# Kernel tuning notes

Measured on AMD Instinct MI355X. Metric: run time of the kernel, lower is better.

The kernel has to match this reference:

```python
import jax, jax.numpy as jnp
import numpy as np

N_NODES = 50000
N_EDGES = 800000
IN_DIM = 128
ATT_DIM = 128
NEG_SLOPE = 0.01  # nn.LeakyReLU default


def setup_inputs() -> dict:
    key = jax.random.key(0)
    ks = jax.random.split(key, 8)
    x = jax.random.normal(ks[0], (N_NODES, IN_DIM), dtype=jnp.float32)
    src_idx = jax.random.randint(ks[1], (N_EDGES,), 0, N_NODES, dtype=jnp.int32)
    dst_idx = jax.random.randint(ks[2], (N_EDGES,), 0, N_NODES, dtype=jnp.int32)
    # small init scale keeps exp(score) numerically tame
    src_w = jax.random.normal(ks[3], (IN_DIM, ATT_DIM), dtype=jnp.float32) * 0.05
    src_b = jnp.zeros((ATT_DIM,), dtype=jnp.float32)
    dst_w = jax.random.normal(ks[4], (IN_DIM, ATT_DIM), dtype=jnp.float32) * 0.05
    dst_b = jnp.zeros((ATT_DIM,), dtype=jnp.float32)
    att_w = jax.random.normal(ks[5], (ATT_DIM, 1), dtype=jnp.float32) * 0.05
    att_b = jnp.zeros((1,), dtype=jnp.float32)
    return {"x": x, "src_idx": src_idx, "dst_idx": dst_idx,
            "src_w": src_w, "src_b": src_b, "dst_w": dst_w, "dst_b": dst_b,
            "att_w": att_w, "att_b": att_b}


def reference(x, src_idx, dst_idx, src_w, src_b, dst_w, dst_b, att_w, att_b):
    n = x.shape[0]
    # 1) mean aggregation of source features onto destinations (copy_u + mean)
    deg = jax.ops.segment_sum(jnp.ones_like(dst_idx, dtype=x.dtype), dst_idx, num_segments=n)
    h_mean = jax.ops.segment_sum(x[src_idx], dst_idx, num_segments=n)
    h_mean = h_mean / jnp.maximum(deg, 1.0)[:, None]
    # 2) attention projections on nodes (dense GEMMs)
    ha_src = x @ src_w + src_b          # [N, att_dim]
    ha_dst = h_mean @ dst_w + dst_b     # [N, att_dim]
    # 3) per-edge u_add_v -> LeakyReLU -> att Linear -> exp
    e = jax.nn.leaky_relu(ha_src[src_idx] + ha_dst[dst_idx], NEG_SLOPE)  # [E, att_dim]
    s = jnp.exp(e @ att_w + att_b)      # [E, 1]
    # 4) edge softmax: normalize by segment sum over destination
    denom = jax.ops.segment_sum(s, dst_idx, num_segments=n)  # [N, 1]
    a = s / denom[dst_idx]              # [E, 1]
    # 5) u_mul_e weighted aggregation (sum)
    out = jax.ops.segment_sum(x[src_idx] * a, dst_idx, num_segments=n)  # [N, in_dim]
    return out
```

## Files before the change

kernel.cpp:

```cpp
#include <hip/hip_runtime.h>
#include <math.h>

#define N_NODES 50000
#define N_EDGES 800000
#define DIM 128
#define NEG_SLOPE 0.01f
#define CAP 64

typedef short v8s __attribute__((ext_vector_type(8)));
typedef float v4f __attribute__((ext_vector_type(4)));

__device__ inline unsigned f2bf2(float a, float b) {
    unsigned ua = __float_as_uint(a);
    unsigned ub = __float_as_uint(b);
    ua = (ua + 0x7fffu + ((ua >> 16) & 1u)) >> 16;
    ub = (ub + 0x7fffu + ((ub >> 16) & 1u)) & 0xffff0000u;
    return ua | ub;
}
__device__ inline float2 bf2f(unsigned u) {
    float2 r;
    r.x = __uint_as_float(u << 16);
    r.y = __uint_as_float(u & 0xffff0000u);
    return r;
}

__global__ __launch_bounds__(256) void k_prepw(
    const float* __restrict__ src_w, const float* __restrict__ dst_w,
    unsigned* __restrict__ whT, int* __restrict__ deg)
{
    int gid = blockIdx.x * 256 + threadIdx.x;
    if (gid < 256 * 64) {
        int n = gid >> 6;
        int kk = gid & 63;
        const float* W = (n < 128) ? src_w : dst_w;
        int col = n & 127;
        float w0 = W[(2 * kk) * DIM + col];
        float w1 = W[(2 * kk + 1) * DIM + col];
        whT[gid] = f2bf2(w0, w1);
    }
    if (gid < N_NODES) deg[gid] = 0;
}

__global__ __launch_bounds__(256) void k_scatter(
    const int* __restrict__ src, const int* __restrict__ dst,
    int* __restrict__ deg, int* __restrict__ slots)
{
    int e = blockIdx.x * 256 + threadIdx.x;
    if (e >= N_EDGES) return;
    int d = dst[e];
    int pos = atomicAdd(&deg[d], 1);
    if (pos < CAP) slots[d * CAP + pos] = src[e] * 64;
}

__global__ __launch_bounds__(256) void k_gemm(
    const float* __restrict__ x, const unsigned* __restrict__ whT,
    const float* __restrict__ src_b, unsigned* __restrict__ hx_u,
    unsigned* __restrict__ yu)
{
    __shared__ unsigned lds[64][196];
    int wave = threadIdx.x >> 6;
    int lane = threadIdx.x & 63;
    int quad = lane >> 4;
    int m = lane & 15;
    int m0 = blockIdx.x * 64 + wave * 16;
    int arow = m0 + m;
    int lr = wave * 16 + m;
    bool live = (arow < N_NODES);

    v8s b[4];
    #pragma unroll
    for (int k0 = 0; k0 < 4; ++k0) {
        float4 f0 = make_float4(0.f, 0.f, 0.f, 0.f);
        float4 f1 = f0;
        if (live) {
            const float4* xp = (const float4*)(x + (size_t)arow * DIM + k0 * 32 + quad * 8);
            f0 = xp[0];
            f1 = xp[1];
        }
        union { unsigned u[4]; v8s s; } pk;
        pk.u[0] = f2bf2(f0.x, f0.y);
        pk.u[1] = f2bf2(f0.z, f0.w);
        pk.u[2] = f2bf2(f1.x, f1.y);
        pk.u[3] = f2bf2(f1.z, f1.w);
        b[k0] = pk.s;
        int c = k0 * 32 + quad * 8 + 1;
        lds[lr][c + 0] = pk.u[0];
        lds[lr][c + 2] = pk.u[1];
        lds[lr][c + 4] = pk.u[2];
        lds[lr][c + 6] = pk.u[3];
    }

    #pragma unroll
    for (int nt = 0; nt < 16; ++nt) {
        v4f acc = {0.f, 0.f, 0.f, 0.f};
        const uint4* ap = (const uint4*)(whT + (size_t)(nt * 16 + m) * 64 + quad * 4);
        #pragma unroll
        for (int k0 = 0; k0 < 4; ++k0) {
            union { uint4 u; v8s s; } af;
            af.u = ap[k0 * 4];
            acc = __builtin_amdgcn_mfma_f32_16x16x32_bf16(af.s, b[k0], acc, 0, 0, 0);
        }
        if (nt < 8) {
            float4 bia = ((const float4*)src_b)[nt * 4 + quad];
            int c = nt * 16 + quad * 4;
            lds[lr][c]     = f2bf2(acc[0] + bia.x, acc[1] + bia.y);
            lds[lr][c + 2] = f2bf2(acc[2] + bia.z, acc[3] + bia.w);
        } else {
            int c = 64 + nt * 8 + quad * 2;
            lds[lr][c]     = f2bf2(acc[0], acc[1]);
            lds[lr][c + 1] = f2bf2(acc[2], acc[3]);
        }
    }
    __syncthreads();

    int rbase = blockIdx.x * 64;
    for (int i = threadIdx.x; i < 64 * 32; i += 256) {
        int r = i >> 5, c = i & 31;
        int row = rbase + r;
        if (row < N_NODES)
            ((uint4*)(hx_u + (size_t)row * 128))[c] = *(const uint4*)&lds[r][c * 4];
    }
    for (int i = threadIdx.x; i < 64 * 16; i += 256) {
        int r = i >> 4, c = i & 15;
        int row = rbase + r;
        if (row < N_NODES)
            ((uint4*)(yu + (size_t)row * 64))[c] = *(const uint4*)&lds[r][128 + c * 4];
    }
}

__global__ __launch_bounds__(256) void k_fuse(
    const uint2* __restrict__ hx, const unsigned* __restrict__ yu,
    const int* __restrict__ slots, const int* __restrict__ deg,
    const float* __restrict__ dst_b, const float* __restrict__ att_w,
    const float* __restrict__ att_b, float* __restrict__ out)
{
    int g = blockIdx.x * 256 + threadIdx.x;
    int node = g >> 6;
    int lane = g & 63;
    int grp = lane >> 4;
    int sl = lane & 15;
    int cnt = deg[node];
    if (cnt == 0) {
        if (grp < 2)
            ((float4*)out)[node * 32 + 2 * sl + grp] = make_float4(0.f, 0.f, 0.f, 0.f);
        return;
    }
    const int* sp = slots + node * CAP;

    float hd[8] = {0.f, 0.f, 0.f, 0.f, 0.f, 0.f, 0.f, 0.f};
    for (int i = grp; i < cnt; i += 4) {
        int off = sp[i];
        uint4 q = *((const uint4*)(yu + off) + sl);
        float2 f;
        f = bf2f(q.x); hd[0] += f.x; hd[1] += f.y;
        f = bf2f(q.y); hd[2] += f.x; hd[3] += f.y;
        f = bf2f(q.z); hd[4] += f.x; hd[5] += f.y;
        f = bf2f(q.w); hd[6] += f.x; hd[7] += f.y;
    }
    float inv = 1.0f / (float)cnt;
    float4 db0 = ((const float4*)dst_b)[2 * sl];
    float4 db1 = ((const float4*)dst_b)[2 * sl + 1];
    #pragma unroll
    for (int j = 0; j < 8; ++j) {
        hd[j] += __shfl_xor(hd[j], 32);
        hd[j] += __shfl_xor(hd[j], 16);
        hd[j] *= inv;
    }
    hd[0] += db0.x; hd[1] += db0.y; hd[2] += db0.z; hd[3] += db0.w;
    hd[4] += db1.x; hd[5] += db1.y; hd[6] += db1.z; hd[7] += db1.w;

    float4 aw0 = ((const float4*)att_w)[2 * sl];
    float4 aw1 = ((const float4*)att_w)[2 * sl + 1];
    float ab = att_b[0];
    float o[8] = {0.f, 0.f, 0.f, 0.f, 0.f, 0.f, 0.f, 0.f};
    float dsum = 0.f;
    for (int i = grp; i < cnt; i += 4) {
        int off = sp[i];
        const uint4* hp = (const uint4*)(hx + off);
        uint4 qa = hp[2 * sl];
        uint4 qb = hp[2 * sl + 1];
        float2 h01 = bf2f(qa.x), h23 = bf2f(qa.z);
        float2 h45 = bf2f(qb.x), h67 = bf2f(qb.z);
        float v, p;
        v = h01.x + hd[0]; v = (v > 0.f) ? v : v * NEG_SLOPE; p  = v * aw0.x;
        v = h01.y + hd[1]; v = (v > 0.f) ? v : v * NEG_SLOPE; p += v * aw0.y;
        v = h23.x + hd[2]; v = (v > 0.f) ? v : v * NEG_SLOPE; p += v * aw0.z;
        v = h23.y + hd[3]; v = (v > 0.f) ? v : v * NEG_SLOPE; p += v * aw0.w;
        v = h45.x + hd[4]; v = (v > 0.f) ? v : v * NEG_SLOPE; p += v * aw1.x;
        v = h45.y + hd[5]; v = (v > 0.f) ? v : v * NEG_SLOPE; p += v * aw1.y;
        v = h67.x + hd[6]; v = (v > 0.f) ? v : v * NEG_SLOPE; p += v * aw1.z;
        v = h67.y + hd[7]; v = (v > 0.f) ? v : v * NEG_SLOPE; p += v * aw1.w;
        p += __shfl_xor(p, 8);
        p += __shfl_xor(p, 4);
        p += __shfl_xor(p, 2);
        p += __shfl_xor(p, 1);
        float s = __expf(p + ab);
        float2 x01 = bf2f(qa.y), x23 = bf2f(qa.w);
        float2 x45 = bf2f(qb.y), x67 = bf2f(qb.w);
        o[0] += s * x01.x; o[1] += s * x01.y;
        o[2] += s * x23.x; o[3] += s * x23.y;
        o[4] += s * x45.x; o[5] += s * x45.y;
        o[6] += s * x67.x; o[7] += s * x67.y;
        dsum += s;
    }
    dsum += __shfl_xor(dsum, 32);
    dsum += __shfl_xor(dsum, 16);
    #pragma unroll
    for (int j = 0; j < 8; ++j) {
        o[j] += __shfl_xor(o[j], 32);
        o[j] += __shfl_xor(o[j], 16);
    }
    float r = 1.0f / dsum;
    if (grp < 2) {
        float4 ov;
        ov.x = o[grp * 4 + 0] * r;
        ov.y = o[grp * 4 + 1] * r;
        ov.z = o[grp * 4 + 2] * r;
        ov.w = o[grp * 4 + 3] * r;
        ((float4*)out)[node * 32 + 2 * sl + grp] = ov;
    }
}

extern "C" void kernel_launch(void* const* d_in, const int* in_sizes, int n_in,
                              void* d_out, int out_size, void* d_ws, size_t ws_size,
                              hipStream_t stream)
{
    const float* x     = (const float*)d_in[0];
    const int*   src   = (const int*)d_in[1];
    const int*   dst   = (const int*)d_in[2];
    const float* src_w = (const float*)d_in[3];
    const float* src_b = (const float*)d_in[4];
    const float* dst_w = (const float*)d_in[5];
    const float* dst_b = (const float*)d_in[6];
    const float* att_w = (const float*)d_in[7];
    const float* att_b = (const float*)d_in[8];
    float* out = (float*)d_out;
    (void)in_sizes; (void)n_in; (void)out_size; (void)ws_size;

    const size_t NF = (size_t)N_NODES * DIM;

    int* ws = (int*)d_ws;
    int* ideg  = ws;
    int* slots = ws + 50048;
    unsigned* whT = (unsigned*)(ws + 3250048);
    unsigned* yu  = whT + 16384;
    uint2*    hx  = (uint2*)(yu + NF / 2);

    k_prepw<<<256, 256, 0, stream>>>(src_w, dst_w, whT, ideg);

    k_scatter<<<N_EDGES / 256, 256, 0, stream>>>(src, dst, ideg, slots);

    k_gemm<<<(N_NODES + 63) / 64, 256, 0, stream>>>(
        x, whT, src_b, (unsigned*)hx, yu);

    k_fuse<<<N_NODES * 64 / 256, 256, 0, stream>>>(
        hx, yu, slots, ideg, dst_b, att_w, att_b, out);
}
```

Measured before the change: 257.3 us.

## Merge scatter and GEMM launches; vectorize fuse kernel with packed math and DPP reductions

The edge-scatter and node GEMM kernels become one launch, with block ranges split by blockIdx, so the two independent stages can overlap and one launch boundary disappears. In the fuse kernel, each lane loads one slot index up front and the loops broadcast it with shuffles instead of re-reading slot memory every iteration. The math uses float2 packed adds/FMAs and fmax-based LeakyReLU, the 16-lane reduction uses DPP row_ror adds, and output stores are nontemporal. Loops are now clamped to CAP, which the old code did not do when reading slots, and the scatter blocks share a kernel whose LDS footprint may reduce their occupancy.

```diff
diff --git a/kernel.cpp b/kernel.cpp
--- a/kernel.cpp
+++ b/kernel.cpp
@@ -6,6 +6,9 @@
 #define DIM 128
 #define NEG_SLOPE 0.01f
 #define CAP 64
+
+#define SCAT_BLOCKS (N_EDGES / 256)
+#define GEMM_BLOCKS ((N_NODES + 63) / 64)
 
 typedef short v8s __attribute__((ext_vector_type(8)));
 typedef float v4f __attribute__((ext_vector_type(4)));
@@ -23,6 +26,20 @@
     r.y = __uint_as_float(u & 0xffff0000u);
     return r;
 }
+
+__device__ inline float2 pka(float2 a, float2 b) {
+    return make_float2(a.x + b.x, a.y + b.y);
+}
+__device__ inline float2 pkfma(float2 a, float2 b, float2 c) {
+    return make_float2(fmaf(a.x, b.x, c.x), fmaf(a.y, b.y, c.y));
+}
+__device__ inline float2 leaky2(float2 v) {
+    return make_float2(fmaxf(v.x, v.x * NEG_SLOPE), fmaxf(v.y, v.y * NEG_SLOPE));
+}
+
+#define ROR_ADD(v, CTRL) \
+    ((v) + __int_as_float(__builtin_amdgcn_update_dpp( \
+        0, __float_as_int(v), (CTRL), 0xf, 0xf, false)))
 
 __global__ __launch_bounds__(256) void k_prepw(
     const float* __restrict__ src_w, const float* __restrict__ dst_w,
@@ -41,28 +58,28 @@
     if (gid < N_NODES) deg[gid] = 0;
 }
 
-__global__ __launch_bounds__(256) void k_scatter(
+__global__ __launch_bounds__(256) void k_scatgemm(
     const int* __restrict__ src, const int* __restrict__ dst,
-    int* __restrict__ deg, int* __restrict__ slots)
-{
-    int e = blockIdx.x * 256 + threadIdx.x;
-    if (e >= N_EDGES) return;
-    int d = dst[e];
-    int pos = atomicAdd(&deg[d], 1);
-    if (pos < CAP) slots[d * CAP + pos] = src[e] * 64;
-}
-
-__global__ __launch_bounds__(256) void k_gemm(
+    int* __restrict__ deg, int* __restrict__ slots,
     const float* __restrict__ x, const unsigned* __restrict__ whT,
     const float* __restrict__ src_b, unsigned* __restrict__ hx_u,
     unsigned* __restrict__ yu)
 {
+    if (blockIdx.x < SCAT_BLOCKS) {
+        int e = blockIdx.x * 256 + threadIdx.x;
+        int d = dst[e];
+        int pos = atomicAdd(&deg[d], 1);
+        if (pos < CAP) slots[d * CAP + pos] = src[e] * 64;
+        return;
+    }
+
     __shared__ unsigned lds[64][196];
+    int bx = blockIdx.x - SCAT_BLOCKS;
     int wave = threadIdx.x >> 6;
     int lane = threadIdx.x & 63;
     int quad = lane >> 4;
     int m = lane & 15;
-    int m0 = blockIdx.x * 64 + wave * 16;
+    int m0 = bx * 64 + wave * 16;
     int arow = m0 + m;
     int lr = wave * 16 + m;
     bool live = (arow < N_NODES);
@@ -113,7 +130,7 @@
     }
     __syncthreads();
 
-    int rbase = blockIdx.x * 64;
+    int rbase = bx * 64;
     for (int i = threadIdx.x; i < 64 * 32; i += 256) {
         int r = i >> 5, c = i & 31;
         int row = rbase + r;
@@ -141,83 +158,92 @@
     int sl = lane & 15;
     int cnt = deg[node];
     if (cnt == 0) {
-        if (grp < 2)
-            ((float4*)out)[node * 32 + 2 * sl + grp] = make_float4(0.f, 0.f, 0.f, 0.f);
+        if (grp < 2) {
+            v4f z = {0.f, 0.f, 0.f, 0.f};
+            __builtin_nontemporal_store(z, (v4f*)out + node * 32 + 2 * sl + grp);
+        }
         return;
     }
-    const int* sp = slots + node * CAP;
-
-    float hd[8] = {0.f, 0.f, 0.f, 0.f, 0.f, 0.f, 0.f, 0.f};
-    for (int i = grp; i < cnt; i += 4) {
-        int off = sp[i];
-        uint4 q = *((const uint4*)(yu + off) + sl);
-        float2 f;
-        f = bf2f(q.x); hd[0] += f.x; hd[1] += f.y;
-        f = bf2f(q.y); hd[2] += f.x; hd[3] += f.y;
-        f = bf2f(q.z); hd[4] += f.x; hd[5] += f.y;
-        f = bf2f(q.w); hd[6] += f.x; hd[7] += f.y;
+    int cc = (cnt < CAP) ? cnt : CAP;
+    int trips = (cc + 3) >> 2;
+    int myoff = (lane < cc) ? slots[node * CAP + lane] : 0;
+
+    float2 hd01 = {0.f, 0.f}, hd23 = {0.f, 0.f};
+    float2 hd45 = {0.f, 0.f}, hd67 = {0.f, 0.f};
+    #pragma unroll 2
+    for (int t = 0; t < trips; ++t) {
+        int i = 4 * t + grp;
+        bool valid = (i < cc);
+        int off = __shfl(myoff, valid ? i : 0);
+        if (valid) {
+            uint4 q = *((const uint4*)(yu + off) + sl);
+            hd01 = pka(hd01, bf2f(q.x));
+            hd23 = pka(hd23, bf2f(q.y));
+            hd45 = pka(hd45, bf2f(q.z));
+            hd67 = pka(hd67, bf2f(q.w));
+        }
     }
     float inv = 1.0f / (float)cnt;
     float4 db0 = ((const float4*)dst_b)[2 * sl];
     float4 db1 = ((const float4*)dst_b)[2 * sl + 1];
-    #pragma unroll
-    for (int j = 0; j < 8; ++j) {
-        hd[j] += __shfl_xor(hd[j], 32);
-        hd[j] += __shfl_xor(hd[j], 16);
-        hd[j] *= inv;
-    }
-    hd[0] += db0.x; hd[1] += db0.y; hd[2] += db0.z; hd[3] += db0.w;
-    hd[4] += db1.x; hd[5] += db1.y; hd[6] += db1.z; hd[7] += db1.w;
+    #define XRED(f) { f += __shfl_xor(f, 32); f += __shfl_xor(f, 16); f *= inv; }
+    XRED(hd01.x) XRED(hd01.y) XRED(hd23.x) XRED(hd23.y)
+    XRED(hd45.x) XRED(hd45.y) XRED(hd67.x) XRED(hd67.y)
+    #undef XRED
+    hd01.x += db0.x; hd01.y += db0.y; hd23.x += db0.z; hd23.y += db0.w;
+    hd45.x += db1.x; hd45.y += db1.y; hd67.x += db1.z; hd67.y += db1.w;
 
     float4 aw0 = ((const float4*)att_w)[2 * sl];
     float4 aw1 = ((const float4*)att_w)[2 * sl + 1];
+    float2 aw01 = make_float2(aw0.x, aw0.y), aw23 = make_float2(aw0.z, aw0.w);
+    float2 aw45 = make_float2(aw1.x, aw1.y), aw67 = make_float2(aw1.z, aw1.w);
     float ab = att_b[0];
-    float o[8] = {0.f, 0.f, 0.f, 0.f, 0.f, 0.f, 0.f, 0.f};
+    float2 o01 = {0.f, 0.f}, o23 = {0.f, 0.f};
+    float2 o45 = {0.f, 0.f}, o67 = {0.f, 0.f};
     float dsum = 0.f;
-    for (int i = grp; i < cnt; i += 4) {
-        int off = sp[i];
-        const uint4* hp = (const uint4*)(hx + off);
-        uint4 qa = hp[2 * sl];
-        uint4 qb = hp[2 * sl + 1];
-        float2 h01 = bf2f(qa.x), h23 = bf2f(qa.z);
-        float2 h45 = bf2f(qb.x), h67 = bf2f(qb.z);
-        float v, p;
-        v = h01.x + hd[0]; v = (v > 0.f) ? v : v * NEG_SLOPE; p  = v * aw0.x;
-        v = h01.y + hd[1]; v = (v > 0.f) ? v : v * NEG_SLOPE; p += v * aw0.y;
-        v = h23.x + hd[2]; v = (v > 0.f) ? v : v * NEG_SLOPE; p += v * aw0.z;
-        v = h23.y + hd[3]; v = (v > 0.f) ? v : v * NEG_SLOPE; p += v * aw0.w;
-        v = h45.x + hd[4]; v = (v > 0.f) ? v : v * NEG_SLOPE; p += v * aw1.x;
-        v = h45.y + hd[5]; v = (v > 0.f) ? v : v * NEG_SLOPE; p += v * aw1.y;
-        v = h67.x + hd[6]; v = (v > 0.f) ? v : v * NEG_SLOPE; p += v * aw1.z;
-        v = h67.y + hd[7]; v = (v > 0.f) ? v : v * NEG_SLOPE; p += v * aw1.w;
-        p += __shfl_xor(p, 8);
-        p += __shfl_xor(p, 4);
-        p += __shfl_xor(p, 2);
-        p += __shfl_xor(p, 1);
-        float s = __expf(p + ab);
-        float2 x01 = bf2f(qa.y), x23 = bf2f(qa.w);
-        float2 x45 = bf2f(qb.y), x67 = bf2f(qb.w);
-        o[0] += s * x01.x; o[1] += s * x01.y;
-        o[2] += s * x23.x; o[3] += s * x23.y;
-        o[4] += s * x45.x; o[5] += s * x45.y;
-        o[6] += s * x67.x; o[7] += s * x67.y;
-        dsum += s;
+    #pragma unroll 2
+    for (int t = 0; t < trips; ++t) {
+        int i = 4 * t + grp;
+        bool valid = (i < cc);
+        int off = __shfl(myoff, valid ? i : 0);
+        if (valid) {
+            const uint4* hp = (const uint4*)(hx + off);
+            uint4 qa = hp[2 * sl];
+            uint4 qb = hp[2 * sl + 1];
+            float2 p2 = {0.f, 0.f};
+            p2 = pkfma(leaky2(pka(bf2f(qa.x), hd01)), aw01, p2);
+            p2 = pkfma(leaky2(pka(bf2f(qa.z), hd23)), aw23, p2);
+            p2 = pkfma(leaky2(pka(bf2f(qb.x), hd45)), aw45, p2);
+            p2 = pkfma(leaky2(pka(bf2f(qb.z), hd67)), aw67, p2);
+            float p = p2.x + p2.y;
+            p = ROR_ADD(p, 0x128);
+            p = ROR_ADD(p, 0x124);
+            p = ROR_ADD(p, 0x122);
+            p = ROR_ADD(p, 0x121);
+            float s = __expf(p + ab);
+            float2 s2 = make_float2(s, s);
+            o01 = pkfma(bf2f(qa.y), s2, o01);
+            o23 = pkfma(bf2f(qa.w), s2, o23);
+            o45 = pkfma(bf2f(qb.y), s2, o45);
+            o67 = pkfma(bf2f(qb.w), s2, o67);
+            dsum += s;
+        }
     }
     dsum += __shfl_xor(dsum, 32);
     dsum += __shfl_xor(dsum, 16);
-    #pragma unroll
-    for (int j = 0; j < 8; ++j) {
-        o[j] += __shfl_xor(o[j], 32);
-        o[j] += __shfl_xor(o[j], 16);
-    }
+    #define XRED2(f) { f += __shfl_xor(f, 32); f += __shfl_xor(f, 16); }
+    XRED2(o01.x) XRED2(o01.y) XRED2(o23.x) XRED2(o23.y)
+    XRED2(o45.x) XRED2(o45.y) XRED2(o67.x) XRED2(o67.y)
+    #undef XRED2
     float r = 1.0f / dsum;
     if (grp < 2) {
-        float4 ov;
-        ov.x = o[grp * 4 + 0] * r;
-        ov.y = o[grp * 4 + 1] * r;
-        ov.z = o[grp * 4 + 2] * r;
-        ov.w = o[grp * 4 + 3] * r;
-        ((float4*)out)[node * 32 + 2 * sl + grp] = ov;
+        v4f ov;
+        if (grp == 0) {
+            ov[0] = o01.x * r; ov[1] = o01.y * r; ov[2] = o23.x * r; ov[3] = o23.y * r;
+        } else {
+            ov[0] = o45.x * r; ov[1] = o45.y * r; ov[2] = o67.x * r; ov[3] = o67.y * r;
+        }
+        __builtin_nontemporal_store(ov, (v4f*)out + node * 32 + 2 * sl + grp);
     }
 }
 
@@ -248,10 +274,8 @@
 
     k_prepw<<<256, 256, 0, stream>>>(src_w, dst_w, whT, ideg);
 
-    k_scatter<<<N_EDGES / 256, 256, 0, stream>>>(src, dst, ideg, slots);
-
-    k_gemm<<<(N_NODES + 63) / 64, 256, 0, stream>>>(
-        x, whT, src_b, (unsigned*)hx, yu);
+    k_scatgemm<<<SCAT_BLOCKS + GEMM_BLOCKS, 256, 0, stream>>>(
+        src, dst, ideg, slots, x, whT, src_b, (unsigned*)hx, yu);
 
     k_fuse<<<N_NODES * 64 / 256, 256, 0, stream>>>(
         hx, yu, slots, ideg, dst_b, att_w, att_b, out);
```

New measurement: 256.7 us. About the same (-0.2%).
